# Performance work log

Measured on AMD Instinct MI355X. Metric: run time of the kernel, lower is better.

The kernel has to match this reference:

```python
import jax, jax.numpy as jnp
import numpy as np

# Dimensions: B walkers, S=2 spins, N=8 electrons/spin, D=256 features, I=4 ions
B, S, N, D, I = 8192, 2, 8, 256, 4


def setup_inputs() -> dict:
    key = jax.random.key(0)
    k1, k2, k3, k4, k5, k6 = jax.random.split(key, 6)
    eq_inputs = jax.random.normal(k1, (B, S * N, D), dtype=jnp.float32)
    r_ei = jax.random.normal(k2, (B, S * N, I, 3), dtype=jnp.float32)
    # Orbital layer params (per spin): linear kernel/bias, isotropic envelope
    W = jax.random.normal(k3, (S, D, N), dtype=jnp.float32) / np.sqrt(D)
    b = jax.random.normal(k4, (S, N), dtype=jnp.float32) * 0.1
    decay = jax.random.uniform(k5, (S, I, N), dtype=jnp.float32, minval=0.5, maxval=1.5)
    pi = jax.random.normal(k6, (S, I, N), dtype=jnp.float32)
    return {"eq_inputs": eq_inputs, "r_ei": r_ei, "W": W, "b": b, "decay": decay, "pi": pi}


def _cofactor_antieq(M):
    """M: (..., n, n) -> (..., n), i-th entry = M[i,0] * C[i,0] * (-1)**i."""
    n = M.shape[-1]
    # rows to keep when deleting row i, for each i: (n, n-1)
    full = np.arange(n)
    idx = jnp.asarray(np.stack([np.delete(full, i) for i in range(n)]))
    # delete col 0, then gather row-subsets -> (..., n, n-1, n-1)
    submats = jnp.take(M[..., 1:], idx, axis=-2)
    signs = jnp.asarray((-1.0) ** full, dtype=M.dtype)
    cof = signs * jnp.linalg.det(submats)  # (..., n)
    return M[..., 0] * cof


def reference(eq_inputs, r_ei, W, b, decay, pi):
    # split into equal spins: (B, S, N, D) and (B, S, N, I, 3)
    h = eq_inputs.reshape(B, S, N, D)
    r = r_ei.reshape(B, S, N, I, 3)
    # linear orbital part: (B, S, N, N_orb)
    lin = jnp.einsum("bsnd,sdk->bsnk", h, W) + b[:, None, :]
    # isotropic exponential envelope: sum_ion pi * exp(-decay * |r_ei|)
    dist = jnp.linalg.norm(r, axis=-1)  # (B, S, N, I)
    env = jnp.einsum("bsnik,sik->bsnk",
                     jnp.exp(-dist[..., None] * decay[:, None, :, :]), pi)
    orbitals = lin * env  # (B, S, N, N) square orbital matrices
    anti = _cofactor_antieq(orbitals)  # (B, S, N)
    out = h * anti[..., None]  # (B, S, N, D)
    return (out[:, 0], out[:, 1])
```

## Files before the change

### kernel.cpp

```cpp
#include <hip/hip_runtime.h>
#include <math.h>


__global__ __launch_bounds__(256, 4)
void orbital_cof_kernel(const float* __restrict__ h_g,
                        const float* __restrict__ r_g,
                        const float* __restrict__ W_g,
                        const float* __restrict__ b_g,
                        const float* __restrict__ dec_g,
                        const float* __restrict__ pi_g,
                        float* __restrict__ out,
                        int nb)
{
    __shared__ float hs[16][264];
    __shared__ float Ms[2][8][8];
    __shared__ float anti_s[16];
    __shared__ float dist_s[64];

    const int t = threadIdx.x;
    const int b = blockIdx.x;
    const int wave = t >> 6;
    const int lane = t & 63;
    const int s  = wave >> 1;
    const int kh = wave & 1;

    float wv[4][4];
    {
        const float* wp = W_g + s * 2048 + lane * 32 + kh * 4;
#pragma unroll
        for (int dd = 0; dd < 4; ++dd) {
            float4 w = *(const float4*)(wp + dd * 8);
            wv[dd][0] = w.x; wv[dd][1] = w.y; wv[dd][2] = w.z; wv[dd][3] = w.w;
        }
    }

    const float4* h4p = (const float4*)(h_g + (size_t)b * 4096);
#pragma unroll
    for (int it = 0; it < 4; ++it) {
        int f4 = t + it * 256;
        int row = f4 >> 6;
        int d4 = (f4 & 63) << 2;
        float4 v = h4p[f4];
        *(float4*)&hs[row][d4] = v;
    }

    if (t < 64) {
        const float* rp = r_g + (size_t)b * 192 + t * 3;
        float x = rp[0], y = rp[1], z = rp[2];
        dist_s[t] = sqrtf(x * x + y * y + z * z);
    }
    __syncthreads();

    float v[32];
#pragma unroll
    for (int n = 0; n < 8; ++n) {
        float4 hv = *(const float4*)&hs[s * 8 + n][lane * 4];
#pragma unroll
        for (int kl = 0; kl < 4; ++kl) {
            float acc;
            acc = hv.x * wv[0][kl];
            acc = fmaf(hv.y, wv[1][kl], acc);
            acc = fmaf(hv.z, wv[2][kl], acc);
            acc = fmaf(hv.w, wv[3][kl], acc);
            v[n * 4 + kl] = acc;
        }
    }

#pragma unroll
    for (int i = 0; i < 16; ++i) {
        float send = (lane & 32) ? v[i] : v[i + 16];
        float recv = __shfl_xor(send, 32);
        v[i] = ((lane & 32) ? v[i + 16] : v[i]) + recv;
    }
#pragma unroll
    for (int i = 0; i < 8; ++i) {
        float send = (lane & 16) ? v[i] : v[i + 8];
        float recv = __shfl_xor(send, 16);
        v[i] = ((lane & 16) ? v[i + 8] : v[i]) + recv;
    }
#pragma unroll
    for (int i = 0; i < 4; ++i) {
        float send = (lane & 8) ? v[i] : v[i + 4];
        float recv = __shfl_xor(send, 8);
        v[i] = ((lane & 8) ? v[i + 4] : v[i]) + recv;
    }
#pragma unroll
    for (int i = 0; i < 2; ++i) {
        float send = (lane & 4) ? v[i] : v[i + 2];
        float recv = __shfl_xor(send, 4);
        v[i] = ((lane & 4) ? v[i + 2] : v[i]) + recv;
    }
    {
        float send = (lane & 2) ? v[0] : v[1];
        float recv = __shfl_xor(send, 2);
        v[0] = ((lane & 2) ? v[1] : v[0]) + recv;
    }
    float tot = v[0] + __shfl_xor(v[0], 1);

    if ((lane & 1) == 0) {
        int idx = lane >> 1;
        int n = idx >> 2;
        int k = kh * 4 + (idx & 3);
        float lin = tot + b_g[s * 8 + k];
        float env = 0.f;
#pragma unroll
        for (int i = 0; i < 4; ++i) {
            float dd = dist_s[s * 32 + n * 4 + i];
            env = fmaf(pi_g[s * 32 + i * 8 + k], __expf(-dd * dec_g[s * 32 + i * 8 + k]), env);
        }
        Ms[s][n][k] = lin * env;
    }
    __syncthreads();

    if (t < 16) {
        int ss = t >> 3;
        int n = t & 7;
        float a[7][7];
#pragma unroll
        for (int i = 0; i < 7; ++i) {
            int src = i + (i >= n);
#pragma unroll
            for (int j = 0; j < 7; ++j) a[i][j] = Ms[ss][src][j + 1];
        }
        float det = 1.f;
#pragma unroll
        for (int kk = 0; kk < 7; ++kk) {
#pragma unroll
            for (int i = kk + 1; i < 7; ++i) {
                bool sw = fabsf(a[i][kk]) > fabsf(a[kk][kk]);
#pragma unroll
                for (int j = kk; j < 7; ++j) {
                    float tk = a[kk][j], ti = a[i][j];
                    a[kk][j] = sw ? ti : tk;
                    a[i][j]  = sw ? tk : ti;
                }
                det = sw ? -det : det;
            }
            float piv = a[kk][kk];
            det *= piv;
            float rp = (piv != 0.f) ? (1.f / piv) : 0.f;
#pragma unroll
            for (int i = kk + 1; i < 7; ++i) {
                float f = a[i][kk] * rp;
#pragma unroll
                for (int j = kk + 1; j < 7; ++j) a[i][j] = fmaf(-f, a[kk][j], a[i][j]);
            }
        }
        float sgn = (n & 1) ? -1.f : 1.f;
        anti_s[t] = Ms[ss][n][0] * sgn * det;
    }
    __syncthreads();

#pragma unroll
    for (int it = 0; it < 4; ++it) {
        int f4 = t + it * 256;
        int row = f4 >> 6;
        int d4 = (f4 & 63) << 2;
        float4 hv = *(const float4*)&hs[row][d4];
        float aa = anti_s[row];
        float4 o = make_float4(hv.x * aa, hv.y * aa, hv.z * aa, hv.w * aa);
        int so = row >> 3;
        int n = row & 7;
        size_t off = (size_t)so * (size_t)nb * 2048 + (size_t)b * 2048 + (size_t)(n * 256 + d4);
        *(float4*)(out + off) = o;
    }
}

extern "C" void kernel_launch(void* const* d_in, const int* in_sizes, int n_in,
                              void* d_out, int out_size, void* d_ws, size_t ws_size,
                              hipStream_t stream) {
    int nb = in_sizes[0] / 4096;
    const float* h_g   = (const float*)d_in[0];
    const float* r_g   = (const float*)d_in[1];
    const float* W_g   = (const float*)d_in[2];
    const float* b_g   = (const float*)d_in[3];
    const float* dec_g = (const float*)d_in[4];
    const float* pi_g  = (const float*)d_in[5];
    orbital_cof_kernel<<<dim3(nb), dim3(256), 0, stream>>>(
        h_g, r_g, W_g, b_g, dec_g, pi_g, (float*)d_out, nb);
}
```

Baseline: 56.43 us.

## Assign one walker per wavefront and keep h in registers instead of LDS

Each 256-thread block now handles four walkers, one per wavefront, instead of one walker per block. Each wave loops over both spins, keeps the h rows in registers for the final scaling rather than staging them in shared memory, and reloads W per spin and half. This removes the large LDS tile and shrinks the grid. In exchange each wave does serial work per walker: two spins, two k-halves, and a determinant computed by only 8 lanes. It also adds several block-wide barriers per spin even though the waves are independent.

New measurement: 63.25 us. 1.12x slower.

```diff
diff --git a/kernel.cpp b/kernel.cpp
--- a/kernel.cpp
+++ b/kernel.cpp
@@ -12,157 +12,150 @@
                         float* __restrict__ out,
                         int nb)
 {
-    __shared__ float hs[16][264];
-    __shared__ float Ms[2][8][8];
-    __shared__ float anti_s[16];
-    __shared__ float dist_s[64];
+    __shared__ float dist_s[4][64];
+    __shared__ float Msw[4][8][8];
+    __shared__ float anti_s[4][8];
 
     const int t = threadIdx.x;
-    const int b = blockIdx.x;
     const int wave = t >> 6;
     const int lane = t & 63;
-    const int s  = wave >> 1;
-    const int kh = wave & 1;
+    const int b = blockIdx.x * 4 + wave;
+    const bool valid = b < nb;
 
-    float wv[4][4];
-    {
-        const float* wp = W_g + s * 2048 + lane * 32 + kh * 4;
-#pragma unroll
-        for (int dd = 0; dd < 4; ++dd) {
-            float4 w = *(const float4*)(wp + dd * 8);
-            wv[dd][0] = w.x; wv[dd][1] = w.y; wv[dd][2] = w.z; wv[dd][3] = w.w;
-        }
-    }
-
-    const float4* h4p = (const float4*)(h_g + (size_t)b * 4096);
-#pragma unroll
-    for (int it = 0; it < 4; ++it) {
-        int f4 = t + it * 256;
-        int row = f4 >> 6;
-        int d4 = (f4 & 63) << 2;
-        float4 v = h4p[f4];
-        *(float4*)&hs[row][d4] = v;
-    }
-
-    if (t < 64) {
-        const float* rp = r_g + (size_t)b * 192 + t * 3;
+    if (valid) {
+        const float* rp = r_g + (size_t)b * 192 + lane * 3;
         float x = rp[0], y = rp[1], z = rp[2];
-        dist_s[t] = sqrtf(x * x + y * y + z * z);
+        dist_s[wave][lane] = sqrtf(x * x + y * y + z * z);
     }
     __syncthreads();
 
-    float v[32];
+    for (int s = 0; s < 2; ++s) {
+        float4 hv[8];
+        if (valid) {
+            const float* hb = h_g + (size_t)b * 4096 + s * 2048 + lane * 4;
 #pragma unroll
-    for (int n = 0; n < 8; ++n) {
-        float4 hv = *(const float4*)&hs[s * 8 + n][lane * 4];
-#pragma unroll
-        for (int kl = 0; kl < 4; ++kl) {
-            float acc;
-            acc = hv.x * wv[0][kl];
-            acc = fmaf(hv.y, wv[1][kl], acc);
-            acc = fmaf(hv.z, wv[2][kl], acc);
-            acc = fmaf(hv.w, wv[3][kl], acc);
-            v[n * 4 + kl] = acc;
-        }
-    }
+            for (int n = 0; n < 8; ++n)
+                hv[n] = *(const float4*)(hb + n * 256);
 
 #pragma unroll
-    for (int i = 0; i < 16; ++i) {
-        float send = (lane & 32) ? v[i] : v[i + 16];
-        float recv = __shfl_xor(send, 32);
-        v[i] = ((lane & 32) ? v[i + 16] : v[i]) + recv;
-    }
+            for (int kh = 0; kh < 2; ++kh) {
+                float wv[4][4];
+                const float* wp = W_g + s * 2048 + lane * 32 + kh * 4;
 #pragma unroll
-    for (int i = 0; i < 8; ++i) {
-        float send = (lane & 16) ? v[i] : v[i + 8];
-        float recv = __shfl_xor(send, 16);
-        v[i] = ((lane & 16) ? v[i + 8] : v[i]) + recv;
-    }
+                for (int dd = 0; dd < 4; ++dd) {
+                    float4 w = *(const float4*)(wp + dd * 8);
+                    wv[dd][0] = w.x; wv[dd][1] = w.y; wv[dd][2] = w.z; wv[dd][3] = w.w;
+                }
+                float v[32];
 #pragma unroll
-    for (int i = 0; i < 4; ++i) {
-        float send = (lane & 8) ? v[i] : v[i + 4];
-        float recv = __shfl_xor(send, 8);
-        v[i] = ((lane & 8) ? v[i + 4] : v[i]) + recv;
-    }
+                for (int n = 0; n < 8; ++n) {
 #pragma unroll
-    for (int i = 0; i < 2; ++i) {
-        float send = (lane & 4) ? v[i] : v[i + 2];
-        float recv = __shfl_xor(send, 4);
-        v[i] = ((lane & 4) ? v[i + 2] : v[i]) + recv;
-    }
-    {
-        float send = (lane & 2) ? v[0] : v[1];
-        float recv = __shfl_xor(send, 2);
-        v[0] = ((lane & 2) ? v[1] : v[0]) + recv;
-    }
-    float tot = v[0] + __shfl_xor(v[0], 1);
+                    for (int kl = 0; kl < 4; ++kl) {
+                        float acc = hv[n].x * wv[0][kl];
+                        acc = fmaf(hv[n].y, wv[1][kl], acc);
+                        acc = fmaf(hv[n].z, wv[2][kl], acc);
+                        acc = fmaf(hv[n].w, wv[3][kl], acc);
+                        v[n * 4 + kl] = acc;
+                    }
+                }
+#pragma unroll
+                for (int i = 0; i < 16; ++i) {
+                    float send = (lane & 32) ? v[i] : v[i + 16];
+                    float recv = __shfl_xor(send, 32);
+                    v[i] = ((lane & 32) ? v[i + 16] : v[i]) + recv;
+                }
+#pragma unroll
+                for (int i = 0; i < 8; ++i) {
+                    float send = (lane & 16) ? v[i] : v[i + 8];
+                    float recv = __shfl_xor(send, 16);
+                    v[i] = ((lane & 16) ? v[i + 8] : v[i]) + recv;
+                }
+#pragma unroll
+                for (int i = 0; i < 4; ++i) {
+                    float send = (lane & 8) ? v[i] : v[i + 4];
+                    float recv = __shfl_xor(send, 8);
+                    v[i] = ((lane & 8) ? v[i + 4] : v[i]) + recv;
+                }
+#pragma unroll
+                for (int i = 0; i < 2; ++i) {
+                    float send = (lane & 4) ? v[i] : v[i + 2];
+                    float recv = __shfl_xor(send, 4);
+                    v[i] = ((lane & 4) ? v[i + 2] : v[i]) + recv;
+                }
+                {
+                    float send = (lane & 2) ? v[0] : v[1];
+                    float recv = __shfl_xor(send, 2);
+                    v[0] = ((lane & 2) ? v[1] : v[0]) + recv;
+                }
+                float tot = v[0] + __shfl_xor(v[0], 1);
 
-    if ((lane & 1) == 0) {
-        int idx = lane >> 1;
-        int n = idx >> 2;
-        int k = kh * 4 + (idx & 3);
-        float lin = tot + b_g[s * 8 + k];
-        float env = 0.f;
+                if ((lane & 1) == 0) {
+                    int idx = lane >> 1;
+                    int n = idx >> 2;
+                    int k = kh * 4 + (idx & 3);
+                    float lin = tot + b_g[s * 8 + k];
+                    float env = 0.f;
 #pragma unroll
-        for (int i = 0; i < 4; ++i) {
-            float dd = dist_s[s * 32 + n * 4 + i];
-            env = fmaf(pi_g[s * 32 + i * 8 + k], __expf(-dd * dec_g[s * 32 + i * 8 + k]), env);
-        }
-        Ms[s][n][k] = lin * env;
-    }
-    __syncthreads();
-
-    if (t < 16) {
-        int ss = t >> 3;
-        int n = t & 7;
-        float a[7][7];
-#pragma unroll
-        for (int i = 0; i < 7; ++i) {
-            int src = i + (i >= n);
-#pragma unroll
-            for (int j = 0; j < 7; ++j) a[i][j] = Ms[ss][src][j + 1];
-        }
-        float det = 1.f;
-#pragma unroll
-        for (int kk = 0; kk < 7; ++kk) {
-#pragma unroll
-            for (int i = kk + 1; i < 7; ++i) {
-                bool sw = fabsf(a[i][kk]) > fabsf(a[kk][kk]);
-#pragma unroll
-                for (int j = kk; j < 7; ++j) {
-                    float tk = a[kk][j], ti = a[i][j];
-                    a[kk][j] = sw ? ti : tk;
-                    a[i][j]  = sw ? tk : ti;
+                    for (int i = 0; i < 4; ++i) {
+                        float dd2 = dist_s[wave][s * 32 + n * 4 + i];
+                        env = fmaf(pi_g[s * 32 + i * 8 + k],
+                                   __expf(-dd2 * dec_g[s * 32 + i * 8 + k]), env);
+                    }
+                    Msw[wave][n][k] = lin * env;
                 }
-                det = sw ? -det : det;
-            }
-            float piv = a[kk][kk];
-            det *= piv;
-            float rp = (piv != 0.f) ? (1.f / piv) : 0.f;
-#pragma unroll
-            for (int i = kk + 1; i < 7; ++i) {
-                float f = a[i][kk] * rp;
-#pragma unroll
-                for (int j = kk + 1; j < 7; ++j) a[i][j] = fmaf(-f, a[kk][j], a[i][j]);
             }
         }
-        float sgn = (n & 1) ? -1.f : 1.f;
-        anti_s[t] = Ms[ss][n][0] * sgn * det;
-    }
-    __syncthreads();
+        __syncthreads();
 
+        if (valid && lane < 8) {
+            int n = lane;
+            float a[7][7];
 #pragma unroll
-    for (int it = 0; it < 4; ++it) {
-        int f4 = t + it * 256;
-        int row = f4 >> 6;
-        int d4 = (f4 & 63) << 2;
-        float4 hv = *(const float4*)&hs[row][d4];
-        float aa = anti_s[row];
-        float4 o = make_float4(hv.x * aa, hv.y * aa, hv.z * aa, hv.w * aa);
-        int so = row >> 3;
-        int n = row & 7;
-        size_t off = (size_t)so * (size_t)nb * 2048 + (size_t)b * 2048 + (size_t)(n * 256 + d4);
-        *(float4*)(out + off) = o;
+            for (int i = 0; i < 7; ++i) {
+                int src = i + (i >= n);
+#pragma unroll
+                for (int j = 0; j < 7; ++j) a[i][j] = Msw[wave][src][j + 1];
+            }
+            float det = 1.f;
+#pragma unroll
+            for (int kk = 0; kk < 7; ++kk) {
+#pragma unroll
+                for (int i = kk + 1; i < 7; ++i) {
+                    bool sw = fabsf(a[i][kk]) > fabsf(a[kk][kk]);
+#pragma unroll
+                    for (int j = kk; j < 7; ++j) {
+                        float tk = a[kk][j], ti = a[i][j];
+                        a[kk][j] = sw ? ti : tk;
+                        a[i][j]  = sw ? tk : ti;
+                    }
+                    det = sw ? -det : det;
+                }
+                float piv = a[kk][kk];
+                det *= piv;
+                float rp = (piv != 0.f) ? (1.f / piv) : 0.f;
+#pragma unroll
+                for (int i = kk + 1; i < 7; ++i) {
+                    float f = a[i][kk] * rp;
+#pragma unroll
+                    for (int j = kk + 1; j < 7; ++j) a[i][j] = fmaf(-f, a[kk][j], a[i][j]);
+                }
+            }
+            float sgn = (n & 1) ? -1.f : 1.f;
+            anti_s[wave][n] = Msw[wave][n][0] * sgn * det;
+        }
+        __syncthreads();
+
+        if (valid) {
+            float* ob = out + (size_t)s * (size_t)nb * 2048 + (size_t)b * 2048 + lane * 4;
+#pragma unroll
+            for (int n = 0; n < 8; ++n) {
+                float aa = anti_s[wave][n];
+                float4 hx = hv[n];
+                float4 o = make_float4(hx.x * aa, hx.y * aa, hx.z * aa, hx.w * aa);
+                *(float4*)(ob + n * 256) = o;
+            }
+        }
+        __syncthreads();
     }
 }
 
@@ -176,6 +169,7 @@
     const float* b_g   = (const float*)d_in[3];
     const float* dec_g = (const float*)d_in[4];
     const float* pi_g  = (const float*)d_in[5];
-    orbital_cof_kernel<<<dim3(nb), dim3(256), 0, stream>>>(
+    int grid = (nb + 3) / 4;
+    orbital_cof_kernel<<<dim3(grid), dim3(256), 0, stream>>>(
         h_g, r_g, W_g, b_g, dec_g, pi_g, (float*)d_out, nb);
 }
```
